# Performance work log

Hardware: AMD Instinct MI355X
Metric: run time of the kernel (lower is better)

## Reference

```python
import jax, jax.numpy as jnp
import numpy as np


def psf2otf(psf, shape):
    """Zero-pad psf to `shape` and circularly shift so its center is at the
    origin, then 2D FFT. psf: [..., kh, kw] -> complex [..., H, W]."""
    kh, kw = psf.shape[-2], psf.shape[-1]
    H, W = shape
    pad = jnp.zeros(psf.shape[:-2] + (H, W), psf.dtype)
    pad = pad.at[..., :kh, :kw].set(psf)
    pad = jnp.roll(pad, shift=(-(kh // 2), -(kw // 2)), axis=(-2, -1))
    return jnp.fft.fft2(pad)


def setup_inputs() -> dict:
    key = jax.random.key(0)
    k1, k2, k3, k4, k5 = jax.random.split(key, 5)
    B, C, H, W = 4, 3, 512, 512
    NF, FS, KS = 24, 5, 25
    y = jax.random.normal(k1, (B, C, H, W), dtype=jnp.float32)
    k = jax.random.uniform(k2, (B, 1, KS, KS), dtype=jnp.float32)
    k = k / jnp.sum(k, axis=(-2, -1), keepdims=True)  # normalized blur PSF
    w = 0.5 + jax.random.uniform(k3, (B, 1), dtype=jnp.float32)  # positive (Softplus output)
    phi = jax.random.normal(k4, (B, C, H, W), dtype=jnp.float32)
    weights = jax.random.normal(k5, (NF, C, FS, FS), dtype=jnp.float32) * 0.3
    return {"y": y, "k": k, "w": w, "phi": phi, "weights": weights}


def reference(y, k, w, phi, weights):
    # FFT-domain Wiener deconvolution (FourierDeconvolutionFunction_init.forward).
    B, C, H, W = y.shape
    Fy = jnp.fft.fft2(y)                         # [B,C,H,W] complex64
    Dg = psf2otf(weights, (H, W))                # [NF,C,H,W] complex64
    Dk = psf2otf(k, (H, W))                      # [B,1,H,W] complex64, broadcasts over C
    w4 = w[:, :, None, None]                     # [B,1,1,1]
    Fphi = jnp.fft.fft2(phi / w4)                # [B,C,H,W]
    Dg_sum = jnp.sum(jnp.abs(Dg) ** 2, axis=0)[None] / w4   # [B,C,H,W] real
    Omega = 1.0 / (jnp.abs(Dk) ** 2 + Dg_sum)    # [B,C,H,W] real
    num = Omega * (jnp.conj(Dk) * Fy + Fphi)     # [B,C,H,W] complex64
    out = jnp.real(jnp.fft.ifft2(num)).astype(y.dtype)  # torch.irfft(..., onesided=False)
    return out
```

## Files before the change

kernel.cpp:

```cpp
#include <hip/hip_runtime.h>
#include <math.h>

#define PI_F 3.14159265358979323846f
#define NPIX 262144

__device__ __forceinline__ float2 cmul(float2 a, float2 b) {
    return make_float2(a.x * b.x - a.y * b.y, a.x * b.y + a.y * b.x);
}
__device__ __forceinline__ float2 cadd(float2 a, float2 b) {
    return make_float2(a.x + b.x, a.y + b.y);
}
__device__ __forceinline__ float2 csub(float2 a, float2 b) {
    return make_float2(a.x - b.x, a.y - b.y);
}

template<int DIR>
__device__ __forceinline__ void fill_tw(float2* tw, int t, int stride) {
    for (int m = t; m < 384; m += stride) {
        const float ang = (2.0f * PI_F / 512.0f) * (float)m;
        const float s = __sinf(ang), c = __cosf(ang);
        tw[m] = make_float2(c, (DIR > 0) ? s : -s);
    }
}

template<int DIR>
__device__ __forceinline__ float2* fft512(float2* sA, float2* sB,
                                          const float2* tw, int t) {
    float2* X = sA;
    float2* Y = sB;
    int Ns = 1;
#pragma unroll
    for (int s = 0; s < 4; ++s) {
        const int jm = t & (Ns - 1);
        const int jd = t - jm;
        float2 v0 = X[t], v1 = X[t + 128], v2 = X[t + 256], v3 = X[t + 384];
        const int m1 = jm * (128 / Ns);
        v1 = cmul(tw[m1], v1);
        v2 = cmul(tw[2 * m1], v2);
        v3 = cmul(tw[3 * m1], v3);
        const float2 t0 = cadd(v0, v2), t1 = csub(v0, v2);
        const float2 t2 = cadd(v1, v3), t3 = csub(v1, v3);
        const float2 t3i = (DIR > 0) ? make_float2(-t3.y, t3.x)
                                     : make_float2(t3.y, -t3.x);
        const int od = (jd << 2) + jm;
        Y[od]          = cadd(t0, t2);
        Y[od + Ns]     = cadd(t1, t3i);
        Y[od + 2 * Ns] = csub(t0, t2);
        Y[od + 3 * Ns] = csub(t1, t3i);
        __syncthreads();
        float2* tmp = X; X = Y; Y = tmp;
        Ns <<= 2;
    }
#pragma unroll
    for (int q = 0; q < 2; ++q) {
        const int j = t + q * 128;
        const float2 a = X[j], b = X[j + 256];
        const float2 tt = cmul(tw[j], b);
        Y[j]       = cadd(a, tt);
        Y[j + 256] = csub(a, tt);
    }
    __syncthreads();
    return Y;
}

__global__ __launch_bounds__(128) void fwd_fft_all(const float* __restrict__ y,
                                                   const float* __restrict__ phi,
                                                   const float* __restrict__ w,
                                                   float2* __restrict__ S) {
    __shared__ float2 sA[512], sB[512], tw[384];
    const int t = threadIdx.x;
    fill_tw<-1>(tw, t, 128);
    if (blockIdx.x < 6144) {
        const int img = blockIdx.x >> 9, row = blockIdx.x & 511;
        const size_t off = (size_t)img * NPIX + (size_t)row * 512;
        const float iwv = 1.0f / w[img / 3];
        const float4 yv = ((const float4*)(y + off))[t];
        const float4 pv = ((const float4*)(phi + off))[t];
        sA[4 * t + 0] = make_float2(yv.x, pv.x * iwv);
        sA[4 * t + 1] = make_float2(yv.y, pv.y * iwv);
        sA[4 * t + 2] = make_float2(yv.z, pv.z * iwv);
        sA[4 * t + 3] = make_float2(yv.w, pv.w * iwv);
        __syncthreads();
        float2* R = fft512<-1>(sA, sB, tw, t);
        float4* wp = (float4*)(S + off);
        for (int k = t; k < 256; k += 128)
            wp[k] = make_float4(R[2 * k].x, R[2 * k].y,
                                R[2 * k + 1].x, R[2 * k + 1].y);
        return;
    }
    const int bid = blockIdx.x - 6144;
    int img, row;
    if (bid < 100) {
        img = 12 + bid / 25;
        row = (bid % 25 - 12) & 511;
    } else {
        const int g = bid - 100;
        img = 16 + g / 9;
        row = ((g % 9) - 4) & 511;
    }
    float2* rp = S + (size_t)img * NPIX + (size_t)row * 512;
    for (int k = t; k < 512; k += 128) sA[k] = rp[k];
    __syncthreads();
    float2* R = fft512<-1>(sA, sB, tw, t);
    for (int k = t; k < 512; k += 128) rp[k] = R[k];
}

template<int DIR>
__global__ __launch_bounds__(1024) void col_fft(const float2* __restrict__ in,
                                                float2* __restrict__ outp) {
    __shared__ float2 sX[8 * 513], sY[8 * 513], tw[384];
    const int t = threadIdx.x;
    const int img = blockIdx.x >> 6;
    const int u0 = (blockIdx.x & 63) << 3;
    fill_tw<DIR>(tw, t, 1024);
    const float2* ip = in + (size_t)img * NPIX + u0;
    for (int f = t; f < 2048; f += 1024) {
        const int row = f >> 2, seg = f & 3;
        const float4 v = *(const float4*)(ip + (size_t)row * 512 + seg * 2);
        sX[(seg * 2)     * 513 + row] = make_float2(v.x, v.y);
        sX[(seg * 2 + 1) * 513 + row] = make_float2(v.z, v.w);
    }
    __syncthreads();
    const int c = t >> 7, tt = t & 127;
    float2* R = fft512<DIR>(sX + c * 513, sY + c * 513, tw, tt);
    float4* wp = (float4*)(outp + (size_t)img * NPIX + (size_t)(u0 + c) * 512);
    for (int k = tt; k < 256; k += 128)
        wp[k] = make_float4(R[2 * k].x, R[2 * k].y,
                            R[2 * k + 1].x, R[2 * k + 1].y);
}

__device__ __forceinline__ float2 get2(const float4 a, const float4 b, int q) {
    switch (q) {
        case 0:  return make_float2(a.x, a.y);
        case 1:  return make_float2(a.z, a.w);
        case 2:  return make_float2(b.x, b.y);
        default: return make_float2(b.z, b.w);
    }
}

__global__ __launch_bounds__(256) void combine_ifft(const float2* __restrict__ T,
                                                    const float* __restrict__ w,
                                                    float2* __restrict__ P) {
    __shared__ float2 sA[2][512], sB[2][512], tw[384];
    __shared__ float2 zrow[2][2][512];
    const int t = threadIdx.x;
    const int h = t >> 7, tt = t & 127;
    const int rr = blockIdx.x;
    const int pair = blockIdx.y;
    const int r0 = rr, r1 = (512 - rr) & 511;
    const int rh = h ? r1 : r0;
    fill_tw<1>(tw, t, 256);
    const int i0 = 2 * pair, i1 = 2 * pair + 1;
    const int b0 = i0 / 3, b1 = i1 / 3;
    const int ch0 = i0 % 3, ch1 = i1 % 3;
    const float iw0 = 1.0f / w[b0], iw1 = 1.0f / w[b1];
    const size_t rowh = (size_t)rh * 512;
    const float4* Zv0 = (const float4*)(T + (size_t)i0 * NPIX + rowh);
    const float4* Zv1 = (const float4*)(T + (size_t)i1 * NPIX + rowh);
    const float4* K0 = (const float4*)(T + (size_t)(12 + b0) * NPIX + rowh);
    const float4* K1 = (const float4*)(T + (size_t)(12 + b1) * NPIX + rowh);
    const float4* G0 = (const float4*)(T + (size_t)(16 + ch0) * NPIX + rowh);
    const float4* G1 = (const float4*)(T + (size_t)(16 + ch1) * NPIX + rowh);

    const float4 za = Zv0[2 * tt], zb = Zv0[2 * tt + 1];
    const float4 ua = Zv1[2 * tt], ub = Zv1[2 * tt + 1];
    const float4 ka = K0[2 * tt],  kb = K0[2 * tt + 1];
    const float4 la = K1[2 * tt],  lb = K1[2 * tt + 1];
    const float4 ga = G0[2 * tt],  gb = G0[2 * tt + 1];
    const float4 ha = G1[2 * tt],  hb = G1[2 * tt + 1];
    zrow[h][0][4 * tt + 0] = make_float2(za.x, za.y);
    zrow[h][0][4 * tt + 1] = make_float2(za.z, za.w);
    zrow[h][0][4 * tt + 2] = make_float2(zb.x, zb.y);
    zrow[h][0][4 * tt + 3] = make_float2(zb.z, zb.w);
    zrow[h][1][4 * tt + 0] = make_float2(ua.x, ua.y);
    zrow[h][1][4 * tt + 1] = make_float2(ua.z, ua.w);
    zrow[h][1][4 * tt + 2] = make_float2(ub.x, ub.y);
    zrow[h][1][4 * tt + 3] = make_float2(ub.z, ub.w);
    __syncthreads();
    const float2* Zm0 = zrow[1 - h][0];
    const float2* Zm1 = zrow[1 - h][1];
#pragma unroll
    for (int q = 0; q < 4; ++q) {
        const int c = 4 * tt + q;
        const int nc = (512 - c) & 511;
        float2 num[2];
#pragma unroll
        for (int e = 0; e < 2; ++e) {
            const float2 Zv = e ? get2(ua, ub, q) : get2(za, zb, q);
            const float2 Zn = e ? Zm1[nc] : Zm0[nc];
            const float2 K  = e ? get2(la, lb, q) : get2(ka, kb, q);
            const float dg  = (e ? get2(ha, hb, q).x : get2(ga, gb, q).x) *
                              (e ? iw1 : iw0);
            const float2 Zm = make_float2(Zn.x, -Zn.y);
            const float2 Fy = make_float2(0.5f * (Zv.x + Zm.x),
                                          0.5f * (Zv.y + Zm.y));
            const float dx = Zv.x - Zm.x, dy = Zv.y - Zm.y;
            const float2 Fphi = make_float2(0.5f * dy, -0.5f * dx);
            const float kk = K.x * K.x + K.y * K.y;
            const float Om = 1.0f / (kk + dg);
            const float2 cf = make_float2(K.x * Fy.x + K.y * Fy.y,
                                          K.x * Fy.y - K.y * Fy.x);
            num[e] = make_float2(Om * (cf.x + Fphi.x), Om * (cf.y + Fphi.y));
        }
        sA[h][c] = make_float2(num[0].x - num[1].y, num[0].y + num[1].x);
    }
    __syncthreads();
    float2* R = fft512<1>(&sA[h][0], &sB[h][0], tw, tt);
    if (!(h == 1 && r1 == r0)) {
        float4* wp = (float4*)(P + (size_t)pair * NPIX + rowh);
        for (int k = tt; k < 256; k += 128)
            wp[k] = make_float4(R[2 * k].x, R[2 * k].y,
                                R[2 * k + 1].x, R[2 * k + 1].y);
    }
}

__global__ __launch_bounds__(1024) void col_ifft_unpack(const float2* __restrict__ P,
                                                        float* __restrict__ out) {
    __shared__ float2 sX[8 * 513], sY[8 * 513], tw[384];
    const int t = threadIdx.x;
    const int pair = blockIdx.x >> 6;
    const int s0 = (blockIdx.x & 63) << 3;
    fill_tw<1>(tw, t, 1024);
    const float2* ip = P + (size_t)pair * NPIX + s0;
    for (int f = t; f < 2048; f += 1024) {
        const int row = f >> 2, seg = f & 3;
        const float4 v = *(const float4*)(ip + (size_t)row * 512 + seg * 2);
        sX[(seg * 2)     * 513 + row] = make_float2(v.x, v.y);
        sX[(seg * 2 + 1) * 513 + row] = make_float2(v.z, v.w);
    }
    __syncthreads();
    const int c = t >> 7, tt = t & 127;
    float2* R = fft512<1>(sX + c * 513, sY + c * 513, tw, tt);
    const float sc = 1.0f / 262144.0f;
    float* o0 = out + (size_t)(2 * pair) * NPIX + (size_t)(s0 + c) * 512;
    float* o1 = o0 + NPIX;
    ((float4*)o0)[tt] = make_float4(R[4 * tt].x * sc, R[4 * tt + 1].x * sc,
                                    R[4 * tt + 2].x * sc, R[4 * tt + 3].x * sc);
    ((float4*)o1)[tt] = make_float4(R[4 * tt].y * sc, R[4 * tt + 1].y * sc,
                                    R[4 * tt + 2].y * sc, R[4 * tt + 3].y * sc);
}

__global__ __launch_bounds__(256) void prep_kg(const float* __restrict__ kin,
                                               const float* __restrict__ wts,
                                               float2* __restrict__ S) {
    const int bid = blockIdx.x, tid = threadIdx.x;
    if (bid < 10) {
        const int t = bid * 256 + tid;
        if (t < 2500) {
            const int b = t / 625, rem = t % 625;
            const int i = rem / 25, j = rem % 25;
            const int r = (i - 12) & 511, c = (j - 12) & 511;
            S[(size_t)(12 + b) * NPIX + (size_t)r * 512 + c] =
                make_float2(kin[t], 0.0f);
        }
        return;
    }
    const int ch = bid - 10;
    __shared__ float gp[24][13][13];
    __shared__ float part[243];
    float* gpf = &gp[0][0][0];
    for (int i = tid; i < 24 * 169; i += 256) gpf[i] = 0.0f;
    __syncthreads();
    for (int i = tid; i < 600; i += 256) {
        const int f = i / 25, rem = i % 25;
        const int x = rem / 5, yy = rem % 5;
        gp[f][x + 4][yy + 4] = wts[(size_t)(f * 3 + ch) * 25 + rem];
    }
    __syncthreads();
    if (tid < 243) {
        const int dpos = tid / 3, seg = tid % 3;
        const int di = dpos / 9 - 4, dj = dpos % 9 - 4;
        float acc = 0.0f;
        for (int f = seg * 8; f < seg * 8 + 8; ++f) {
#pragma unroll
            for (int x = 0; x < 5; ++x)
#pragma unroll
                for (int yy = 0; yy < 5; ++yy)
                    acc += gp[f][x + 4][yy + 4] *
                           gp[f][x + di + 4][yy + dj + 4];
        }
        part[tid] = acc;
    }
    __syncthreads();
    if (tid < 81) {
        const float a = part[tid * 3] + part[tid * 3 + 1] + part[tid * 3 + 2];
        const int di = tid / 9 - 4, dj = tid % 9 - 4;
        const int r = di & 511, c = dj & 511;
        S[(size_t)(16 + ch) * NPIX + (size_t)r * 512 + c] =
            make_float2(a, 0.0f);
    }
}

extern "C" void kernel_launch(void* const* d_in, const int* in_sizes, int n_in,
                              void* d_out, int out_size, void* d_ws, size_t ws_size,
                              hipStream_t stream) {
    const float* y   = (const float*)d_in[0];
    const float* k   = (const float*)d_in[1];
    const float* w   = (const float*)d_in[2];
    const float* phi = (const float*)d_in[3];
    const float* wts = (const float*)d_in[4];
    float* out = (float*)d_out;

    const size_t needed = (size_t)38 * NPIX * sizeof(float2);
    if (ws_size < needed) return;
    float2* S = (float2*)d_ws;
    float2* T = S + (size_t)19 * NPIX;
    float2* P = S;

    hipMemsetAsync(S + (size_t)12 * NPIX, 0,
                   (size_t)7 * NPIX * sizeof(float2), stream);

    prep_kg<<<13, 256, 0, stream>>>(k, wts, S);
    fwd_fft_all<<<6271, 128, 0, stream>>>(y, phi, w, S);

    col_fft<-1><<<19 * 64, 1024, 0, stream>>>(S, T);

    combine_ifft<<<dim3(257, 6), 256, 0, stream>>>(T, w, P);

    col_ifft_unpack<<<6 * 64, 1024, 0, stream>>>(P, out);
}
```

Before: 144.7 us.

## Drop workspace memset; build sparse PSF rows in shared memory and skip zero rows

Removes the 7-image memset of the PSF and filter-autocorrelation planes. The row-FFT blocks now build their nonzero rows directly in shared memory from the kernel and autocorrelation inputs, and the autocorrelation moves into a tiny separate kernel. The column FFT skips global loads for rows known to be zero in the sparse planes and fills them with zeros instead. This cuts a large memset (about 14 MB) and the matching zero-row reads, at the cost of an extra small launch and some branch logic.

```diff
diff --git a/kernel.cpp b/kernel.cpp
--- a/kernel.cpp
+++ b/kernel.cpp
@@ -63,9 +63,44 @@
     return Y;
 }
 
+__global__ __launch_bounds__(256) void autocorr3(const float* __restrict__ wts,
+                                                 float* __restrict__ A3) {
+    const int ch = blockIdx.x, tid = threadIdx.x;
+    __shared__ float gp[24][13][13];
+    __shared__ float part[243];
+    float* gpf = &gp[0][0][0];
+    for (int i = tid; i < 24 * 169; i += 256) gpf[i] = 0.0f;
+    __syncthreads();
+    for (int i = tid; i < 600; i += 256) {
+        const int f = i / 25, rem = i % 25;
+        const int x = rem / 5, yy = rem % 5;
+        gp[f][x + 4][yy + 4] = wts[(size_t)(f * 3 + ch) * 25 + rem];
+    }
+    __syncthreads();
+    if (tid < 243) {
+        const int dpos = tid / 3, seg = tid % 3;
+        const int di = dpos / 9 - 4, dj = dpos % 9 - 4;
+        float acc = 0.0f;
+        for (int f = seg * 8; f < seg * 8 + 8; ++f) {
+#pragma unroll
+            for (int x = 0; x < 5; ++x)
+#pragma unroll
+                for (int yy = 0; yy < 5; ++yy)
+                    acc += gp[f][x + 4][yy + 4] *
+                           gp[f][x + di + 4][yy + dj + 4];
+        }
+        part[tid] = acc;
+    }
+    __syncthreads();
+    if (tid < 81)
+        A3[ch * 81 + tid] = part[tid * 3] + part[tid * 3 + 1] + part[tid * 3 + 2];
+}
+
 __global__ __launch_bounds__(128) void fwd_fft_all(const float* __restrict__ y,
                                                    const float* __restrict__ phi,
                                                    const float* __restrict__ w,
+                                                   const float* __restrict__ kin,
+                                                   const float* __restrict__ A3,
                                                    float2* __restrict__ S) {
     __shared__ float2 sA[512], sB[512], tw[384];
     const int t = threadIdx.x;
@@ -90,18 +125,25 @@
     }
     const int bid = blockIdx.x - 6144;
     int img, row;
+    for (int k = t; k < 512; k += 128) sA[k] = make_float2(0.0f, 0.0f);
+    __syncthreads();
     if (bid < 100) {
-        img = 12 + bid / 25;
-        row = (bid % 25 - 12) & 511;
+        const int b = bid / 25, i = bid % 25;
+        img = 12 + b;
+        row = (i - 12) & 511;
+        if (t < 25)
+            sA[(t - 12) & 511] = make_float2(kin[b * 625 + i * 25 + t], 0.0f);
     } else {
         const int g = bid - 100;
-        img = 16 + g / 9;
-        row = ((g % 9) - 4) & 511;
-    }
+        const int ch = g / 9, di = g % 9;
+        img = 16 + ch;
+        row = (di - 4) & 511;
+        if (t < 9)
+            sA[(t - 4) & 511] = make_float2(A3[ch * 81 + di * 9 + t], 0.0f);
+    }
+    __syncthreads();
+    float2* R = fft512<-1>(sA, sB, tw, t);
     float2* rp = S + (size_t)img * NPIX + (size_t)row * 512;
-    for (int k = t; k < 512; k += 128) sA[k] = rp[k];
-    __syncthreads();
-    float2* R = fft512<-1>(sA, sB, tw, t);
     for (int k = t; k < 512; k += 128) rp[k] = R[k];
 }
 
@@ -114,9 +156,14 @@
     const int u0 = (blockIdx.x & 63) << 3;
     fill_tw<DIR>(tw, t, 1024);
     const float2* ip = in + (size_t)img * NPIX + u0;
+    const int sh  = (img >= 16) ? 4 : 12;
+    const int lim = (img >= 16) ? 9 : 25;
+    const bool sparse = (img >= 12);
     for (int f = t; f < 2048; f += 1024) {
         const int row = f >> 2, seg = f & 3;
-        const float4 v = *(const float4*)(ip + (size_t)row * 512 + seg * 2);
+        float4 v = make_float4(0.0f, 0.0f, 0.0f, 0.0f);
+        if (!sparse || (((row + sh) & 511) < lim))
+            v = *(const float4*)(ip + (size_t)row * 512 + seg * 2);
         sX[(seg * 2)     * 513 + row] = make_float2(v.x, v.y);
         sX[(seg * 2 + 1) * 513 + row] = make_float2(v.z, v.w);
     }
@@ -240,57 +287,6 @@
                                     R[4 * tt + 2].y * sc, R[4 * tt + 3].y * sc);
 }
 
-__global__ __launch_bounds__(256) void prep_kg(const float* __restrict__ kin,
-                                               const float* __restrict__ wts,
-                                               float2* __restrict__ S) {
-    const int bid = blockIdx.x, tid = threadIdx.x;
-    if (bid < 10) {
-        const int t = bid * 256 + tid;
-        if (t < 2500) {
-            const int b = t / 625, rem = t % 625;
-            const int i = rem / 25, j = rem % 25;
-            const int r = (i - 12) & 511, c = (j - 12) & 511;
-            S[(size_t)(12 + b) * NPIX + (size_t)r * 512 + c] =
-                make_float2(kin[t], 0.0f);
-        }
-        return;
-    }
-    const int ch = bid - 10;
-    __shared__ float gp[24][13][13];
-    __shared__ float part[243];
-    float* gpf = &gp[0][0][0];
-    for (int i = tid; i < 24 * 169; i += 256) gpf[i] = 0.0f;
-    __syncthreads();
-    for (int i = tid; i < 600; i += 256) {
-        const int f = i / 25, rem = i % 25;
-        const int x = rem / 5, yy = rem % 5;
-        gp[f][x + 4][yy + 4] = wts[(size_t)(f * 3 + ch) * 25 + rem];
-    }
-    __syncthreads();
-    if (tid < 243) {
-        const int dpos = tid / 3, seg = tid % 3;
-        const int di = dpos / 9 - 4, dj = dpos % 9 - 4;
-        float acc = 0.0f;
-        for (int f = seg * 8; f < seg * 8 + 8; ++f) {
-#pragma unroll
-            for (int x = 0; x < 5; ++x)
-#pragma unroll
-                for (int yy = 0; yy < 5; ++yy)
-                    acc += gp[f][x + 4][yy + 4] *
-                           gp[f][x + di + 4][yy + dj + 4];
-        }
-        part[tid] = acc;
-    }
-    __syncthreads();
-    if (tid < 81) {
-        const float a = part[tid * 3] + part[tid * 3 + 1] + part[tid * 3 + 2];
-        const int di = tid / 9 - 4, dj = tid % 9 - 4;
-        const int r = di & 511, c = dj & 511;
-        S[(size_t)(16 + ch) * NPIX + (size_t)r * 512 + c] =
-            make_float2(a, 0.0f);
-    }
-}
-
 extern "C" void kernel_launch(void* const* d_in, const int* in_sizes, int n_in,
                               void* d_out, int out_size, void* d_ws, size_t ws_size,
                               hipStream_t stream) {
@@ -301,17 +297,15 @@
     const float* wts = (const float*)d_in[4];
     float* out = (float*)d_out;
 
-    const size_t needed = (size_t)38 * NPIX * sizeof(float2);
+    const size_t needed = (size_t)38 * NPIX * sizeof(float2) + 4096;
     if (ws_size < needed) return;
     float2* S = (float2*)d_ws;
     float2* T = S + (size_t)19 * NPIX;
+    float*  A3 = (float*)(T + (size_t)19 * NPIX);
     float2* P = S;
 
-    hipMemsetAsync(S + (size_t)12 * NPIX, 0,
-                   (size_t)7 * NPIX * sizeof(float2), stream);
-
-    prep_kg<<<13, 256, 0, stream>>>(k, wts, S);
-    fwd_fft_all<<<6271, 128, 0, stream>>>(y, phi, w, S);
+    autocorr3<<<3, 256, 0, stream>>>(wts, A3);
+    fwd_fft_all<<<6271, 128, 0, stream>>>(y, phi, w, k, A3, S);
 
     col_fft<-1><<<19 * 64, 1024, 0, stream>>>(S, T);
 
```

After: 138.9 us. 4.0% less time.
